# Kernel tuning notes

Hardware: AMD Instinct MI355X
Metric: run time of the kernel (lower is better)

The kernel has to match this reference:

```python
import jax, jax.numpy as jnp
import numpy as np

N = 100000
E = 1200000


def _gcn_norm(edge_index, num_nodes):
    # Add self-loops and compute symmetric normalization (PyG GCNConv default).
    row = jnp.concatenate([edge_index[0], jnp.arange(num_nodes, dtype=edge_index.dtype)])
    col = jnp.concatenate([edge_index[1], jnp.arange(num_nodes, dtype=edge_index.dtype)])
    deg = jax.ops.segment_sum(jnp.ones_like(col, dtype=jnp.float32), col, num_segments=num_nodes)
    dinv = jnp.where(deg > 0, jax.lax.rsqrt(jnp.maximum(deg, 1.0)), 0.0)
    norm = dinv[row] * dinv[col]  # [E+N]
    return row, col, norm


def _gcn_conv(x, W, b, row, col, norm, num_nodes):
    h = x @ W                      # [N, out] dense transform first (fewer bytes to gather)
    msg = h[row] * norm[:, None]   # gather + edge-wise scale
    out = jax.ops.segment_sum(msg, col, num_segments=num_nodes)  # scatter-add to targets
    return out + b


def setup_inputs() -> dict:
    key = jax.random.key(0)
    k1, k2, k3, k4 = jax.random.split(key, 4)
    x = jax.random.normal(k1, (N, 128), dtype=jnp.float32)
    edge_index = jax.random.randint(k2, (2, E), 0, N, dtype=jnp.int64)
    W1 = jax.random.normal(k3, (128, 256), dtype=jnp.float32) * (1.0 / np.sqrt(128))
    b1 = jnp.zeros((256,), dtype=jnp.float32)
    W2 = jax.random.normal(k4, (256, 40), dtype=jnp.float32) * (1.0 / np.sqrt(256))
    b2 = jnp.zeros((40,), dtype=jnp.float32)
    return {"x": x, "edge_index": edge_index, "W1": W1, "b1": b1, "W2": W2, "b2": b2}


def reference(x, edge_index, W1, b1, W2, b2):
    row, col, norm = _gcn_norm(edge_index, N)
    h = _gcn_conv(x, W1, b1, row, col, norm, N)
    h = jax.nn.relu(h)
    # dropout omitted: eval mode (training=False) is identity
    return _gcn_conv(h, W2, b2, row, col, norm, N)
```

## Files before the change

kernel.cpp:

```cpp
#include <hip/hip_runtime.h>
#include <hip/hip_bf16.h>

#define NN 100000
#define EE 1200000
#define F1 128
#define F2 256
#define F3 40
#define MROWS 64
#define NBUK ((NN + 255) / 256)
#define NBLK 256
#define CHUNK ((EE + NBLK - 1) / NBLK)
#define DCAP 4096
#define XB2 ((NN * 32 + 255) / 256)

typedef __bf16 bf16x8 __attribute__((ext_vector_type(8)));
typedef float  f32x4  __attribute__((ext_vector_type(4)));

__device__ __forceinline__ unsigned short f2bf(float f) {
    unsigned u = __float_as_uint(f);
    return (unsigned short)((u + 0x7fffu + ((u >> 16) & 1u)) >> 16);
}
__device__ __forceinline__ float bflo(unsigned v) { return __uint_as_float(v << 16); }
__device__ __forceinline__ float bfhi(unsigned v) { return __uint_as_float(v & 0xffff0000u); }

__global__ __launch_bounds__(256) void k_scatA(const int* __restrict__ row,
                                               const int* __restrict__ col,
                                               int* __restrict__ bcur,
                                               unsigned* __restrict__ rec) {
    __shared__ int lh[NBUK];
    __shared__ int lbase[NBUK];
    for (int i = threadIdx.x; i < NBUK; i += 256) lh[i] = 0;
    __syncthreads();
    const int e0 = blockIdx.x * CHUNK;
    const int e1 = min(e0 + CHUNK, EE);
    for (int e = e0 + threadIdx.x; e < e1; e += 256) {
        int c = col[e];
        if ((unsigned)c < (unsigned)NN) atomicAdd(&lh[c >> 8], 1);
    }
    __syncthreads();
    for (int i = threadIdx.x; i < NBUK; i += 256) {
        int cn = lh[i];
        lbase[i] = cn ? atomicAdd(&bcur[i], cn) : 0;
        lh[i] = 0;
    }
    __syncthreads();
    for (int e = e0 + threadIdx.x; e < e1; e += 256) {
        int r = row[e], c = col[e];
        if ((unsigned)c < (unsigned)NN) {
            int b = c >> 8;
            int pos = lbase[b] + atomicAdd(&lh[b], 1);
            if (pos < DCAP)
                rec[(size_t)b * DCAP + pos] =
                    ((unsigned)r & 0xFFFFFFu) | ((unsigned)(c & 255) << 24);
        }
    }
}

__global__ __launch_bounds__(256) void k_csr(const int* __restrict__ bcur,
                                             const unsigned* __restrict__ rec,
                                             int* __restrict__ eidx,
                                             int* __restrict__ cnt,
                                             int* __restrict__ cursor,
                                             float* __restrict__ dinv) {
    __shared__ int lcnt[256];
    __shared__ int s[256];
    __shared__ int lcur[256];
    __shared__ unsigned lrec[DCAP];
    __shared__ int lde[DCAP];
    const int b = blockIdx.x;
    const int tid = threadIdx.x;
    lcnt[tid] = 0;
    __syncthreads();
    const int base = b * DCAP;
    const int nb = min(bcur[b], DCAP);
    for (int j = tid; j < nb; j += 256) {
        unsigned v = rec[(size_t)base + j];
        lrec[j] = v;
        atomicAdd(&lcnt[v >> 24], 1);
    }
    __syncthreads();
    int cv = lcnt[tid];
    s[tid] = cv;
    __syncthreads();
    int acc = cv;
    for (int d = 1; d < 256; d <<= 1) {
        int add = (tid >= d) ? s[tid - d] : 0;
        __syncthreads();
        acc += add;
        s[tid] = acc;
        __syncthreads();
    }
    int excl = acc - cv;
    lcur[tid] = excl;
    const int node = (b << 8) + tid;
    if (node < NN) {
        cnt[node] = cv;
        cursor[node] = base + excl + cv;
        dinv[node] = rsqrtf((float)(cv + 1));
    }
    __syncthreads();
    for (int j = tid; j < nb; j += 256) {
        unsigned v = lrec[j];
        int pos = atomicAdd(&lcur[v >> 24], 1);
        lde[pos] = (int)(v & 0xFFFFFFu);
    }
    __syncthreads();
    for (int j = tid; j < nb; j += 256) eidx[base + j] = lde[j];
}

__global__ void k_prep(const float4* __restrict__ x, const float* __restrict__ dinv,
                       uint2* __restrict__ xh,
                       const float* __restrict__ W1, const float* __restrict__ W2,
                       __hip_bfloat16* __restrict__ W1p, __hip_bfloat16* __restrict__ W2p) {
    if (blockIdx.x < XB2) {
        int idx = blockIdx.x * 256 + threadIdx.x;
        float d = dinv[idx >> 5];
        float4 v = x[idx];
        uint2 o;
        o.x = (unsigned)f2bf(v.x * d) | ((unsigned)f2bf(v.y * d) << 16);
        o.y = (unsigned)f2bf(v.z * d) | ((unsigned)f2bf(v.w * d) << 16);
        xh[idx] = o;
    } else {
        int idx = (blockIdx.x - XB2) * 256 + threadIdx.x;
        if (idx < F1 * F2) {
            int k = idx / F2, col = idx - (idx / F2) * F2;
            int k8 = k >> 3, j = k & 7;
            W1p[((size_t)(k8 * F2 + col) << 3) + j] = __float2bfloat16(W1[(size_t)k * F2 + col]);
        } else if (idx < F1 * F2 + F2 * 48) {
            int i2 = idx - F1 * F2;
            int k = i2 / 48, col = i2 - (i2 / 48) * 48;
            int k8 = k >> 3, j = k & 7;
            float v = (col < F3) ? W2[(size_t)k * F3 + col] : 0.0f;
            W2p[((size_t)(k8 * 48 + col) << 3) + j] = __float2bfloat16(v);
        }
    }
}

__global__ __launch_bounds__(256) void k_agg1(const int* __restrict__ cursor,
                                              const int* __restrict__ cnt,
                                              const int* __restrict__ eidx,
                                              const float* __restrict__ dinv,
                                              const unsigned* __restrict__ xh,
                                              unsigned* __restrict__ agg) {
    int node = blockIdx.x * 4 + (threadIdx.x >> 6);
    int lane = threadIdx.x & 63;
    if (node >= NN) return;
    unsigned vs = xh[((size_t)node << 6) + lane];
    float a0 = bflo(vs), a1 = bfhi(vs);
    int n = cnt[node];
    int s = cursor[node] - n;
    int k = 0;
    for (; k + 7 < n; k += 8) {
        int r0 = eidx[s + k + 0], r1 = eidx[s + k + 1];
        int r2 = eidx[s + k + 2], r3 = eidx[s + k + 3];
        int r4 = eidx[s + k + 4], r5 = eidx[s + k + 5];
        int r6 = eidx[s + k + 6], r7 = eidx[s + k + 7];
        unsigned v0 = xh[((size_t)r0 << 6) + lane];
        unsigned v1 = xh[((size_t)r1 << 6) + lane];
        unsigned v2 = xh[((size_t)r2 << 6) + lane];
        unsigned v3 = xh[((size_t)r3 << 6) + lane];
        unsigned v4 = xh[((size_t)r4 << 6) + lane];
        unsigned v5 = xh[((size_t)r5 << 6) + lane];
        unsigned v6 = xh[((size_t)r6 << 6) + lane];
        unsigned v7 = xh[((size_t)r7 << 6) + lane];
        a0 += bflo(v0); a1 += bfhi(v0);
        a0 += bflo(v1); a1 += bfhi(v1);
        a0 += bflo(v2); a1 += bfhi(v2);
        a0 += bflo(v3); a1 += bfhi(v3);
        a0 += bflo(v4); a1 += bfhi(v4);
        a0 += bflo(v5); a1 += bfhi(v5);
        a0 += bflo(v6); a1 += bfhi(v6);
        a0 += bflo(v7); a1 += bfhi(v7);
    }
    for (; k + 3 < n; k += 4) {
        int r0 = eidx[s + k + 0], r1 = eidx[s + k + 1];
        int r2 = eidx[s + k + 2], r3 = eidx[s + k + 3];
        unsigned v0 = xh[((size_t)r0 << 6) + lane];
        unsigned v1 = xh[((size_t)r1 << 6) + lane];
        unsigned v2 = xh[((size_t)r2 << 6) + lane];
        unsigned v3 = xh[((size_t)r3 << 6) + lane];
        a0 += bflo(v0); a1 += bfhi(v0);
        a0 += bflo(v1); a1 += bfhi(v1);
        a0 += bflo(v2); a1 += bfhi(v2);
        a0 += bflo(v3); a1 += bfhi(v3);
    }
    for (; k < n; ++k) {
        unsigned v0 = xh[((size_t)eidx[s + k] << 6) + lane];
        a0 += bflo(v0); a1 += bfhi(v0);
    }
    float d = dinv[node];
    agg[((size_t)node << 6) + lane] = (unsigned)f2bf(a0 * d) | ((unsigned)f2bf(a1 * d) << 16);
}

__global__ __launch_bounds__(256) void k_gemm_mfma(
    const __hip_bfloat16* __restrict__ agg, const __hip_bfloat16* __restrict__ W1p,
    const float* __restrict__ b1, const __hip_bfloat16* __restrict__ W2p,
    const float* __restrict__ dinv, unsigned short* __restrict__ tg) {
    __shared__ __hip_bfloat16 h_s[MROWS][F2 + 8];
    const int i0   = blockIdx.x * MROWS;
    const int wave = threadIdx.x >> 6;
    const int lane = threadIdx.x & 63;
    const int m = lane & 15, q = lane >> 4;
    const int rowA = i0 + wave * 16 + m;

    f32x4 acc[16];
#pragma unroll
    for (int c = 0; c < 16; ++c) acc[c] = (f32x4){0.f, 0.f, 0.f, 0.f};

#pragma unroll
    for (int s = 0; s < 4; ++s) {
        bf16x8 a;
#pragma unroll
        for (int j = 0; j < 8; ++j) a[j] = (__bf16)0.0f;
        if (rowA < NN) a = *(const bf16x8*)(agg + (size_t)rowA * F1 + s * 32 + q * 8);
        const __hip_bfloat16* bp = W1p + ((size_t)(4 * s + q) * F2) * 8;
#pragma unroll
        for (int c = 0; c < 16; ++c) {
            bf16x8 b = *(const bf16x8*)(bp + ((size_t)(c * 16 + m) << 3));
            acc[c] = __builtin_amdgcn_mfma_f32_16x16x32_bf16(a, b, acc[c], 0, 0, 0);
        }
    }

#pragma unroll
    for (int c = 0; c < 16; ++c) {
        int col = c * 16 + m;
        float bj = b1[col];
#pragma unroll
        for (int r = 0; r < 4; ++r) {
            int lr = wave * 16 + q * 4 + r;
            h_s[lr][col] = __float2bfloat16(fmaxf(acc[c][r] + bj, 0.0f));
        }
    }
    __syncthreads();

    f32x4 acc2[3];
#pragma unroll
    for (int c = 0; c < 3; ++c) acc2[c] = (f32x4){0.f, 0.f, 0.f, 0.f};

#pragma unroll
    for (int s = 0; s < 8; ++s) {
        bf16x8 a = *(const bf16x8*)(&h_s[wave * 16 + m][s * 32 + q * 8]);
        const __hip_bfloat16* bp = W2p + ((size_t)(4 * s + q) * 48) * 8;
#pragma unroll
        for (int c = 0; c < 3; ++c) {
            bf16x8 b = *(const bf16x8*)(bp + ((size_t)(c * 16 + m) << 3));
            acc2[c] = __builtin_amdgcn_mfma_f32_16x16x32_bf16(a, b, acc2[c], 0, 0, 0);
        }
    }

#pragma unroll
    for (int c = 0; c < 3; ++c) {
        int col = c * 16 + m;
        if (col < F3) {
#pragma unroll
            for (int r = 0; r < 4; ++r) {
                int grow = i0 + wave * 16 + q * 4 + r;
                if (grow < NN)
                    tg[(size_t)grow * F3 + col] = f2bf(acc2[c][r] * dinv[grow]);
            }
        }
    }
}

__global__ __launch_bounds__(256) void k_agg2(const int* __restrict__ cursor,
                                              const int* __restrict__ cnt,
                                              const int* __restrict__ eidx,
                                              const float* __restrict__ dinv,
                                              const unsigned short* __restrict__ tg,
                                              const float* __restrict__ b2,
                                              float* __restrict__ out) {
    const int wave = threadIdx.x >> 6;
    const int lane = threadIdx.x & 63;
    const int h = lane >> 5;
    const int t = lane & 31;
    const int node = blockIdx.x * 8 + wave * 2 + h;
    const unsigned* __restrict__ tgw = (const unsigned*)tg;
    if (t >= 20) return;

    unsigned vs = tgw[(size_t)node * 20 + t];
    float a0 = bflo(vs), a1 = bfhi(vs);
    const int n = cnt[node];
    const int s = cursor[node] - n;
    int k = 0;
    for (; k + 7 < n; k += 8) {
        int r0 = eidx[s + k + 0], r1 = eidx[s + k + 1];
        int r2 = eidx[s + k + 2], r3 = eidx[s + k + 3];
        int r4 = eidx[s + k + 4], r5 = eidx[s + k + 5];
        int r6 = eidx[s + k + 6], r7 = eidx[s + k + 7];
        unsigned v0 = tgw[(size_t)r0 * 20 + t];
        unsigned v1 = tgw[(size_t)r1 * 20 + t];
        unsigned v2 = tgw[(size_t)r2 * 20 + t];
        unsigned v3 = tgw[(size_t)r3 * 20 + t];
        unsigned v4 = tgw[(size_t)r4 * 20 + t];
        unsigned v5 = tgw[(size_t)r5 * 20 + t];
        unsigned v6 = tgw[(size_t)r6 * 20 + t];
        unsigned v7 = tgw[(size_t)r7 * 20 + t];
        a0 += bflo(v0); a1 += bfhi(v0);
        a0 += bflo(v1); a1 += bfhi(v1);
        a0 += bflo(v2); a1 += bfhi(v2);
        a0 += bflo(v3); a1 += bfhi(v3);
        a0 += bflo(v4); a1 += bfhi(v4);
        a0 += bflo(v5); a1 += bfhi(v5);
        a0 += bflo(v6); a1 += bfhi(v6);
        a0 += bflo(v7); a1 += bfhi(v7);
    }
    for (; k + 3 < n; k += 4) {
        int r0 = eidx[s + k + 0], r1 = eidx[s + k + 1];
        int r2 = eidx[s + k + 2], r3 = eidx[s + k + 3];
        unsigned v0 = tgw[(size_t)r0 * 20 + t];
        unsigned v1 = tgw[(size_t)r1 * 20 + t];
        unsigned v2 = tgw[(size_t)r2 * 20 + t];
        unsigned v3 = tgw[(size_t)r3 * 20 + t];
        a0 += bflo(v0); a1 += bfhi(v0);
        a0 += bflo(v1); a1 += bfhi(v1);
        a0 += bflo(v2); a1 += bfhi(v2);
        a0 += bflo(v3); a1 += bfhi(v3);
    }
    for (; k < n; ++k) {
        unsigned v0 = tgw[(size_t)eidx[s + k] * 20 + t];
        a0 += bflo(v0); a1 += bfhi(v0);
    }
    float d = dinv[node];
    float2 bb = ((const float2*)b2)[t];
    float2 o;
    o.x = a0 * d + bb.x;
    o.y = a1 * d + bb.y;
    ((float2*)(out + (size_t)node * F3))[t] = o;
}

extern "C" void kernel_launch(void* const* d_in, const int* in_sizes, int n_in,
                              void* d_out, int out_size, void* d_ws, size_t ws_size,
                              hipStream_t stream) {
    const float* x  = (const float*)d_in[0];
    const int*   ei = (const int*)d_in[1];
    const float* W1 = (const float*)d_in[2];
    const float* b1 = (const float*)d_in[3];
    const float* W2 = (const float*)d_in[4];
    const float* b2 = (const float*)d_in[5];
    float* out = (float*)d_out;

    const int* row = ei;
    const int* col = ei + EE;

    int* cnt     = (int*)d_ws;
    int* cursor  = cnt + NN;
    float* dinv  = (float*)(cursor + NN);
    int* bcur    = (int*)(dinv + NN);
    int* eidx    = bcur + NBUK + 9;
    unsigned* xh  = (unsigned*)(eidx + NBUK * DCAP);
    unsigned* agg = xh + (size_t)NN * 64;
    unsigned* rec = agg;
    unsigned short* tg = (unsigned short*)xh;
    __hip_bfloat16* W1p = (__hip_bfloat16*)(agg + (size_t)NN * 64);
    __hip_bfloat16* W2p = W1p + (size_t)F1 * F2;

    hipMemsetAsync(bcur, 0, NBUK * sizeof(int), stream);
    k_scatA<<<NBLK, 256, 0, stream>>>(row, col, bcur, rec);
    k_csr  <<<NBUK, 256, 0, stream>>>(bcur, rec, eidx, cnt, cursor, dinv);

    k_prep<<<XB2 + (F1 * F2 + F2 * 48 + 255) / 256, 256, 0, stream>>>(
        (const float4*)x, dinv, (uint2*)xh, W1, W2, W1p, W2p);

    k_agg1<<<(NN + 3) / 4, 256, 0, stream>>>(cursor, cnt, eidx, dinv, xh, agg);
    k_gemm_mfma<<<(NN + MROWS - 1) / MROWS, 256, 0, stream>>>(
        (const __hip_bfloat16*)agg, W1p, b1, W2p, dinv, tg);
    k_agg2<<<NN / 8, 256, 0, stream>>>(cursor, cnt, eidx, dinv, tg, b2, out);
}
```

Before: 277.4 us.

## Fuse x/weight bf16 prep into CSR kernel and cache edges in LDS during scatter

The separate prep kernel is removed. Each CSR bucket block now scales its 256 nodes' x rows by dinv, taken from shared memory, and writes bf16. Extra blocks appended to the CSR grid handle the weight packing. The scatter kernel now reads row and col only once, staging packed records and bucket ids in shared memory for the second pass instead of re-reading global memory. This saves one launch and one edge re-read, but CSR blocks do more work each and hold more LDS, which can lower occupancy.

```diff
diff --git a/kernel.cpp b/kernel.cpp
--- a/kernel.cpp
+++ b/kernel.cpp
@@ -11,7 +11,7 @@
 #define NBLK 256
 #define CHUNK ((EE + NBLK - 1) / NBLK)
 #define DCAP 4096
-#define XB2 ((NN * 32 + 255) / 256)
+#define WB ((F1 * F2 + F2 * 48 + 255) / 256)
 
 typedef __bf16 bf16x8 __attribute__((ext_vector_type(8)));
 typedef float  f32x4  __attribute__((ext_vector_type(4)));
@@ -29,13 +29,23 @@
                                                unsigned* __restrict__ rec) {
     __shared__ int lh[NBUK];
     __shared__ int lbase[NBUK];
+    __shared__ unsigned lrec[CHUNK];
+    __shared__ unsigned short lbuk[CHUNK];
     for (int i = threadIdx.x; i < NBUK; i += 256) lh[i] = 0;
     __syncthreads();
     const int e0 = blockIdx.x * CHUNK;
-    const int e1 = min(e0 + CHUNK, EE);
-    for (int e = e0 + threadIdx.x; e < e1; e += 256) {
-        int c = col[e];
-        if ((unsigned)c < (unsigned)NN) atomicAdd(&lh[c >> 8], 1);
+    const int ne = min(CHUNK, EE - e0);
+    for (int j = threadIdx.x; j < ne; j += 256) {
+        int e = e0 + j;
+        int r = row[e], c = col[e];
+        if ((unsigned)c < (unsigned)NN) {
+            int b = c >> 8;
+            lbuk[j] = (unsigned short)b;
+            lrec[j] = ((unsigned)r & 0xFFFFFFu) | ((unsigned)(c & 255) << 24);
+            atomicAdd(&lh[b], 1);
+        } else {
+            lbuk[j] = 0xFFFFu;
+        }
     }
     __syncthreads();
     for (int i = threadIdx.x; i < NBUK; i += 256) {
@@ -44,14 +54,11 @@
         lh[i] = 0;
     }
     __syncthreads();
-    for (int e = e0 + threadIdx.x; e < e1; e += 256) {
-        int r = row[e], c = col[e];
-        if ((unsigned)c < (unsigned)NN) {
-            int b = c >> 8;
+    for (int j = threadIdx.x; j < ne; j += 256) {
+        int b = lbuk[j];
+        if (b != 0xFFFF) {
             int pos = lbase[b] + atomicAdd(&lh[b], 1);
-            if (pos < DCAP)
-                rec[(size_t)b * DCAP + pos] =
-                    ((unsigned)r & 0xFFFFFFu) | ((unsigned)(c & 255) << 24);
+            if (pos < DCAP) rec[(size_t)b * DCAP + pos] = lrec[j];
         }
     }
 }
@@ -61,14 +68,36 @@
                                              int* __restrict__ eidx,
                                              int* __restrict__ cnt,
                                              int* __restrict__ cursor,
-                                             float* __restrict__ dinv) {
+                                             float* __restrict__ dinv,
+                                             const float4* __restrict__ x,
+                                             uint2* __restrict__ xh,
+                                             const float* __restrict__ W1,
+                                             const float* __restrict__ W2,
+                                             __hip_bfloat16* __restrict__ W1p,
+                                             __hip_bfloat16* __restrict__ W2p) {
+    const int b = blockIdx.x;
+    const int tid = threadIdx.x;
+    if (b >= NBUK) {
+        int idx = (b - NBUK) * 256 + tid;
+        if (idx < F1 * F2) {
+            int k = idx / F2, c = idx - (idx / F2) * F2;
+            int k8 = k >> 3, j = k & 7;
+            W1p[((size_t)(k8 * F2 + c) << 3) + j] = __float2bfloat16(W1[(size_t)k * F2 + c]);
+        } else {
+            int i2 = idx - F1 * F2;
+            int k = i2 / 48, c = i2 - (i2 / 48) * 48;
+            int k8 = k >> 3, j = k & 7;
+            float v = (c < F3) ? W2[(size_t)k * F3 + c] : 0.0f;
+            W2p[((size_t)(k8 * 48 + c) << 3) + j] = __float2bfloat16(v);
+        }
+        return;
+    }
     __shared__ int lcnt[256];
     __shared__ int s[256];
     __shared__ int lcur[256];
+    __shared__ float ldv[256];
     __shared__ unsigned lrec[DCAP];
     __shared__ int lde[DCAP];
-    const int b = blockIdx.x;
-    const int tid = threadIdx.x;
     lcnt[tid] = 0;
     __syncthreads();
     const int base = b * DCAP;
@@ -93,10 +122,12 @@
     int excl = acc - cv;
     lcur[tid] = excl;
     const int node = (b << 8) + tid;
+    float dv = rsqrtf((float)(cv + 1));
+    ldv[tid] = dv;
     if (node < NN) {
         cnt[node] = cv;
         cursor[node] = base + excl + cv;
-        dinv[node] = rsqrtf((float)(cv + 1));
+        dinv[node] = dv;
     }
     __syncthreads();
     for (int j = tid; j < nb; j += 256) {
@@ -106,33 +137,17 @@
     }
     __syncthreads();
     for (int j = tid; j < nb; j += 256) eidx[base + j] = lde[j];
-}
-
-__global__ void k_prep(const float4* __restrict__ x, const float* __restrict__ dinv,
-                       uint2* __restrict__ xh,
-                       const float* __restrict__ W1, const float* __restrict__ W2,
-                       __hip_bfloat16* __restrict__ W1p, __hip_bfloat16* __restrict__ W2p) {
-    if (blockIdx.x < XB2) {
-        int idx = blockIdx.x * 256 + threadIdx.x;
-        float d = dinv[idx >> 5];
-        float4 v = x[idx];
+
+    const int nnodes = min(256, NN - (b << 8));
+    const float4* xb = x + ((size_t)(b << 8) << 5);
+    uint2* xhb = xh + ((size_t)(b << 8) << 5);
+    for (int j = tid; j < nnodes * 32; j += 256) {
+        float d = ldv[j >> 5];
+        float4 v = xb[j];
         uint2 o;
         o.x = (unsigned)f2bf(v.x * d) | ((unsigned)f2bf(v.y * d) << 16);
         o.y = (unsigned)f2bf(v.z * d) | ((unsigned)f2bf(v.w * d) << 16);
-        xh[idx] = o;
-    } else {
-        int idx = (blockIdx.x - XB2) * 256 + threadIdx.x;
-        if (idx < F1 * F2) {
-            int k = idx / F2, col = idx - (idx / F2) * F2;
-            int k8 = k >> 3, j = k & 7;
-            W1p[((size_t)(k8 * F2 + col) << 3) + j] = __float2bfloat16(W1[(size_t)k * F2 + col]);
-        } else if (idx < F1 * F2 + F2 * 48) {
-            int i2 = idx - F1 * F2;
-            int k = i2 / 48, col = i2 - (i2 / 48) * 48;
-            int k8 = k >> 3, j = k & 7;
-            float v = (col < F3) ? W2[(size_t)k * F3 + col] : 0.0f;
-            W2p[((size_t)(k8 * 48 + col) << 3) + j] = __float2bfloat16(v);
-        }
+        xhb[j] = o;
     }
 }
 
@@ -356,10 +371,9 @@
 
     hipMemsetAsync(bcur, 0, NBUK * sizeof(int), stream);
     k_scatA<<<NBLK, 256, 0, stream>>>(row, col, bcur, rec);
-    k_csr  <<<NBUK, 256, 0, stream>>>(bcur, rec, eidx, cnt, cursor, dinv);
-
-    k_prep<<<XB2 + (F1 * F2 + F2 * 48 + 255) / 256, 256, 0, stream>>>(
-        (const float4*)x, dinv, (uint2*)xh, W1, W2, W1p, W2p);
+    k_csr  <<<NBUK + WB, 256, 0, stream>>>(bcur, rec, eidx, cnt, cursor, dinv,
+                                           (const float4*)x, (uint2*)xh,
+                                           W1, W2, W1p, W2p);
 
     k_agg1<<<(NN + 3) / 4, 256, 0, stream>>>(cursor, cnt, eidx, dinv, xh, agg);
     k_gemm_mfma<<<(NN + MROWS - 1) / MROWS, 256, 0, stream>>>(
```

New measurement: 278.6 us. Within noise of the previous version (+0.4%).
